# Kernel optimization log

Hardware: AMD Instinct MI355X
Metric: run time of the kernel (lower is better)

The kernel has to match this reference:

```python
import jax, jax.numpy as jnp
import numpy as np

B, N, D, T, M, V, K, HB, FF, L, H = 64, 32, 512, 8, 20, 512, 8, 16, 2048, 2, 8
SCALE = 1.0 / np.sqrt(D // H)


def _ln(x, g, b, eps=1e-5):
    m = x.mean(-1, keepdims=True)
    v = ((x - m) ** 2).mean(-1, keepdims=True)
    return (x - m) / jnp.sqrt(v + eps) * g + b


def _heads(x):
    return x.reshape(x.shape[:-1] + (H, D // H))


def setup_inputs():
    ks = iter(jax.random.split(jax.random.key(0), 60))
    def rn(shape, s=1.0):
        return jax.random.normal(next(ks), shape, jnp.float32) * s
    d = {}
    d['ego_query'] = rn((B, 1, D))
    d['agents_query'] = rn((B, N, D))
    d['bev_feature'] = rn((B, D, HB, HB))
    d['agent_states'] = rn((B, N, 8)) * 10.0
    d['agent_labels'] = rn((B, N))
    d['gt_traj'] = rn((B, T, 3))
    d['codebook'] = rn((V, 2), 0.1)
    for p in ['ego_ctx', 'bevproj', 'agent']:
        d[p + '_w'] = rn((D, D), 0.02); d[p + '_b'] = jnp.zeros((D,))
        d[p + '_g'] = jnp.ones((D,)); d[p + '_beta'] = jnp.zeros((D,))
    d['tok_emb'] = rn((V, D), 0.02)
    d['step_e'] = rn((T, D), 0.02)
    d['mode_e'] = rn((M, D), 0.02)
    d['role_e'] = rn((2, D), 0.02)
    d['bos_e'] = rn((1, D), 0.02)
    for p in ['t', 'e', 'v']:
        d[p + '_qkv_w'] = rn((L, 3 * D, D), 0.02); d[p + '_qkv_b'] = jnp.zeros((L, 3 * D))
        d[p + '_out_w'] = rn((L, D, D), 0.02); d[p + '_out_b'] = jnp.zeros((L, D))
        d[p + '_g'] = jnp.ones((L, D)); d[p + '_beta'] = jnp.zeros((L, D))
    d['ffn_w1'] = rn((L, FF, D), 0.02); d['ffn_b1'] = jnp.zeros((L, FF))
    d['ffn_w2'] = rn((L, D, FF), 0.02); d['ffn_b2'] = jnp.zeros((L, D))
    d['ffn_g'] = jnp.ones((L, D)); d['ffn_beta'] = jnp.zeros((L, D))
    d['head_w'] = rn((V, D), 0.02); d['head_b'] = jnp.zeros((V,))
    return d


def reference(ego_query, agents_query, bev_feature, agent_states, agent_labels, gt_traj, codebook,
              ego_ctx_w, ego_ctx_b, ego_ctx_g, ego_ctx_beta,
              bevproj_w, bevproj_b, bevproj_g, bevproj_beta,
              agent_w, agent_b, agent_g, agent_beta,
              tok_emb, step_e, mode_e, role_e, bos_e,
              t_qkv_w, t_qkv_b, t_out_w, t_out_b, t_g, t_beta,
              e_qkv_w, e_qkv_b, e_out_w, e_out_b, e_g, e_beta,
              v_qkv_w, v_qkv_b, v_out_w, v_out_b, v_g, v_beta,
              ffn_w1, ffn_b1, ffn_w2, ffn_b2, ffn_g, ffn_beta,
              head_w, head_b):
    Bd = ego_query.shape[0]
    P = HB * HB
    # BEV tokens [B, P, D]
    bev = jnp.transpose(bev_feature.reshape(Bd, D, P), (0, 2, 1))
    bev = jax.nn.relu(_ln(bev @ bevproj_w.T + bevproj_b, bevproj_g, bevproj_beta))
    # top-K nearest valid agents
    valid = jax.nn.sigmoid(agent_labels) > 0.05
    dist = jnp.where(valid, jnp.linalg.norm(agent_states[..., :2], axis=-1), jnp.inf)
    _, idx = jax.lax.top_k(-dist, K)
    topk_valid = jnp.take_along_axis(valid, idx, axis=1)
    agent_ctx = jnp.take_along_axis(agents_query, idx[..., None], axis=1)  # [B,K,D]
    agent_enc = jax.nn.relu(_ln(agent_ctx @ agent_w.T + agent_b, agent_g, agent_beta))
    agent_kv = agent_enc[:, :, None, :] + step_e[None, None] + role_e[1][None, None, None]  # [B,K,T,D]
    ego_base = jax.nn.relu(_ln(ego_query[:, 0] @ ego_ctx_w.T + ego_ctx_b, ego_ctx_g, ego_ctx_beta))
    # sequential codebook matching (accumulated-position NN scan, no grad)
    gt_pos = jnp.broadcast_to(gt_traj[:, None, :, :2], (Bd, M, T, 2))
    cb = jax.lax.stop_gradient(codebook)
    def cb_step(acc, pos_t):
        dsq = ((acc[:, :, None, :] + cb[None, None] - pos_t[:, :, None, :]) ** 2).sum(-1)  # [B,M,V]
        ii = jnp.argmin(dsq, axis=-1)
        return acc + cb[ii], ii
    _, idxs = jax.lax.scan(cb_step, jnp.zeros((Bd, M, 2), gt_pos.dtype),
                           jnp.moveaxis(jax.lax.stop_gradient(gt_pos), 2, 0))
    tokens = jnp.transpose(idxs, (1, 2, 0))  # [B,M,T]
    # teacher-forced input embeddings
    bos = bos_e[0][None, :] + ego_base  # [B,D]
    inp = jnp.concatenate([jnp.broadcast_to(bos[:, None, None, :], (Bd, M, 1, D)),
                           tok_emb[tokens[:, :, :-1]]], axis=2)
    ego_q = inp + step_e[None, None] + role_e[0][None, None, None] + mode_e[None, :, None, :]
    caus = jnp.triu(jnp.full((T, T), -jnp.inf, ego_q.dtype), 1)
    inv = ~topk_valid
    inv = inv & ~inv.all(axis=-1, keepdims=True)  # guard: never mask everything
    for i in range(L):
        # temporal causal self-attention over T
        qw, kw, vw = jnp.split(t_qkv_w[i], 3, 0); qb, kb, vb = jnp.split(t_qkv_b[i], 3, 0)
        Q, Kh, Vh = _heads(ego_q @ qw.T + qb), _heads(ego_q @ kw.T + kb), _heads(ego_q @ vw.T + vb)
        s = jnp.einsum('bmqhe,bmkhe->bmhqk', Q, Kh) * SCALE + caus
        o = jnp.einsum('bmhqk,bmkhe->bmqhe', jax.nn.softmax(s, -1), Vh).reshape(ego_q.shape)
        ego_q = _ln(ego_q + o @ t_out_w[i].T + t_out_b[i], t_g[i], t_beta[i])
        # ego-to-agent cross-attention (kv varies per step t)
        qw, kw, vw = jnp.split(e_qkv_w[i], 3, 0); qb, kb, vb = jnp.split(e_qkv_b[i], 3, 0)
        Q = _heads(ego_q @ qw.T + qb)  # [B,M,T,H,e]
        Kh, Vh = _heads(agent_kv @ kw.T + kb), _heads(agent_kv @ vw.T + vb)  # [B,K,T,H,e]
        s = jnp.einsum('bmthe,bkthe->bmhtk', Q, Kh) * SCALE
        s = jnp.where(inv[:, None, None, None, :], -jnp.inf, s)
        o = jnp.einsum('bmhtk,bkthe->bmthe', jax.nn.softmax(s, -1), Vh).reshape(ego_q.shape)
        ego_q = _ln(ego_q + o @ e_out_w[i].T + e_out_b[i], e_g[i], e_beta[i])
        # BEV cross-attention
        qw, kw, vw = jnp.split(v_qkv_w[i], 3, 0); qb, kb, vb = jnp.split(v_qkv_b[i], 3, 0)
        Q = _heads(ego_q @ qw.T + qb)
        Kh, Vh = _heads(bev @ kw.T + kb), _heads(bev @ vw.T + vb)  # [B,P,H,e]
        s = jnp.einsum('bmthe,bphe->bmhtp', Q, Kh) * SCALE
        o = jnp.einsum('bmhtp,bphe->bmthe', jax.nn.softmax(s, -1), Vh).reshape(ego_q.shape)
        ego_q = _ln(ego_q + o @ v_out_w[i].T + v_out_b[i], v_g[i], v_beta[i])
        # FFN
        hid = jax.nn.gelu(ego_q @ ffn_w1[i].T + ffn_b1[i], approximate=False)
        ego_q = _ln(ego_q + hid @ ffn_w2[i].T + ffn_b2[i], ffn_g[i], ffn_beta[i])
    return ego_q @ head_w.T + head_b  # token logits [B,M,T,V]
```

## Files before the change

### kernel.cpp

```cpp
#include <hip/hip_runtime.h>
#include <hip/hip_bf16.h>
#include <math.h>
#include <type_traits>

typedef __hip_bfloat16 bf16;
typedef __attribute__((ext_vector_type(8))) short bf16x8;
typedef __attribute__((ext_vector_type(4))) float f32x4;

__device__ __forceinline__ float b2f(bf16 x){ return __bfloat162float(x); }
__device__ __forceinline__ short f2s(float f){
  bf16 h = __float2bfloat16(f);
  short s; __builtin_memcpy(&s, &h, 2); return s;
}
__device__ __forceinline__ float u2f(unsigned short u){ union { unsigned int i; float f; } z; z.i = ((unsigned int)u) << 16; return z.f; }
__device__ __forceinline__ float lo2f(unsigned int u){ union { unsigned int i; float f; } z; z.i = u << 16; return z.f; }
__device__ __forceinline__ float hi2f(unsigned int u){ union { unsigned int i; float f; } z; z.i = u & 0xffff0000u; return z.f; }
__device__ __forceinline__ bf16x8 cvt8(float4 a, float4 b){
  return (bf16x8){f2s(a.x),f2s(a.y),f2s(a.z),f2s(a.w), f2s(b.x),f2s(b.y),f2s(b.z),f2s(b.w)};
}

template<typename AT, typename CT, int ACT, int BN, int RES>
__global__ __launch_bounds__(256, BN == 64 ? 2 : 1)
void k_gemm_mfma(const AT* __restrict__ A, const float* __restrict__ W,
                 const float* __restrict__ bias, CT* C,
                 const float* Rres, int rows, int Kd, int Nc)
{
  __shared__ short As[128][40];
  __shared__ short Bs[BN][40];
  constexpr int NI = BN / 32;
  int rb = blockIdx.x * 128, nb = blockIdx.y * BN;
  int tid = threadIdx.x;
  int l = tid & 63, w = tid >> 6;
  int wr = (w >> 1) * 64, wc = (w & 1) * (BN/2);
  int lr = l & 15, lk = l >> 4;
  f32x4 acc[4][NI];
  #pragma unroll
  for (int i = 0; i < 4; i++)
    #pragma unroll
    for (int j = 0; j < NI; j++)
      acc[i][j] = (f32x4){0.f, 0.f, 0.f, 0.f};
  int sr = tid >> 1;
  int sc = (tid & 1) * 16;
  bool doB = (BN == 128) || (tid < 128);
  bool doA = (rb + sr) < rows;

  float4 faA[4], fbA[4], faB[4], fbB[4];
  bf16x8 baA[2], baB[2];
  #pragma unroll
  for (int i = 0; i < 4; i++){ faA[i] = (float4){0,0,0,0}; fbA[i] = (float4){0,0,0,0};
                               faB[i] = (float4){0,0,0,0}; fbB[i] = (float4){0,0,0,0}; }
  baA[0] = baA[1] = baB[0] = baB[1] = (bf16x8){0,0,0,0,0,0,0,0};

  auto LOADS = [&](float4* fa, bf16x8* ba, float4* fb, int k0){
    if constexpr (std::is_same<AT, float>::value){
      if (doA){
        const float4* p = (const float4*)(A + (size_t)(rb + sr)*Kd + k0 + sc);
        fa[0] = p[0]; fa[1] = p[1]; fa[2] = p[2]; fa[3] = p[3];
      }
    } else {
      if (doA){
        const bf16x8* p = (const bf16x8*)((const unsigned short*)A + (size_t)(rb + sr)*Kd + k0 + sc);
        ba[0] = p[0]; ba[1] = p[1];
      }
    }
    if (doB){
      const float4* p = (const float4*)(W + (size_t)(nb + sr)*Kd + k0 + sc);
      fb[0] = p[0]; fb[1] = p[1]; fb[2] = p[2]; fb[3] = p[3];
    }
  };
  auto STOREK = [&](float4* fa, bf16x8* ba, float4* fb){
    if constexpr (std::is_same<AT, float>::value){
      *(bf16x8*)&As[sr][sc]     = cvt8(fa[0], fa[1]);
      *(bf16x8*)&As[sr][sc + 8] = cvt8(fa[2], fa[3]);
    } else {
      *(bf16x8*)&As[sr][sc]     = ba[0];
      *(bf16x8*)&As[sr][sc + 8] = ba[1];
    }
    if (doB){
      *(bf16x8*)&Bs[sr][sc]     = cvt8(fb[0], fb[1]);
      *(bf16x8*)&Bs[sr][sc + 8] = cvt8(fb[2], fb[3]);
    }
  };
  auto COMPUTE = [&](){
    bf16x8 af[4], bf_[NI];
    #pragma unroll
    for (int mi = 0; mi < 4; mi++) af[mi]  = *(const bf16x8*)&As[wr + mi*16 + lr][lk*8];
    #pragma unroll
    for (int ni = 0; ni < NI; ni++) bf_[ni] = *(const bf16x8*)&Bs[wc + ni*16 + lr][lk*8];
    #pragma unroll
    for (int mi = 0; mi < 4; mi++)
      #pragma unroll
      for (int ni = 0; ni < NI; ni++)
        acc[mi][ni] = __builtin_amdgcn_mfma_f32_16x16x32_bf16(af[mi], bf_[ni], acc[mi][ni], 0, 0, 0);
  };

  int nst = Kd >> 5;
  LOADS(faA, baA, fbA, 0);
  LOADS(faB, baB, fbB, 32);
  for (int s = 0; s < nst; s += 2){
    __syncthreads();
    STOREK(faA, baA, fbA);
    __syncthreads();
    if (s + 2 < nst) LOADS(faA, baA, fbA, (s+2)*32);
    COMPUTE();
    __syncthreads();
    STOREK(faB, baB, fbB);
    __syncthreads();
    if (s + 3 < nst) LOADS(faB, baB, fbB, (s+3)*32);
    COMPUTE();
  }

  #pragma unroll
  for (int mi = 0; mi < 4; mi++){
    #pragma unroll
    for (int ni = 0; ni < NI; ni++){
      int col = nb + wc + ni*16 + lr;
      float bs = bias[col];
      #pragma unroll
      for (int r = 0; r < 4; r++){
        int row = rb + wr + mi*16 + lk*4 + r;
        if (row < rows){
          float v = acc[mi][ni][r] + bs;
          if (RES) v += Rres[(size_t)row*Nc + col];
          if (ACT == 1) v = 0.5f*v*(1.0f + erff(v*0.70710678118654752f));
          if constexpr (std::is_same<CT, float>::value) C[(size_t)row*Nc + col] = v;
          else C[(size_t)row*Nc + col] = __float2bfloat16(v);
        }
      }
    }
  }
}

template<typename XT, typename OT>
__global__ __launch_bounds__(256) void k_ln(const XT* X, const float* R,
                                            const float* g, const float* bt,
                                            OT* out, int relu)
{
  __shared__ float red[4];
  int row = blockIdx.x, t = threadIdx.x;
  size_t base = (size_t)row * 512;
  float x0, x1;
  if constexpr (std::is_same<XT, float>::value){ x0 = X[base + t]; x1 = X[base + t + 256]; }
  else { x0 = b2f(X[base + t]); x1 = b2f(X[base + t + 256]); }
  if (R){ x0 += R[base + t]; x1 += R[base + t + 256]; }
  float v = x0 + x1;
  #pragma unroll
  for (int o = 32; o > 0; o >>= 1) v += __shfl_xor(v, o);
  if ((t & 63) == 0) red[t >> 6] = v;
  __syncthreads();
  float mean = (red[0]+red[1]+red[2]+red[3]) * (1.0f/512.0f);
  float d0 = x0 - mean, d1 = x1 - mean;
  v = d0*d0 + d1*d1;
  #pragma unroll
  for (int o = 32; o > 0; o >>= 1) v += __shfl_xor(v, o);
  __syncthreads();
  if ((t & 63) == 0) red[t >> 6] = v;
  __syncthreads();
  float var = (red[0]+red[1]+red[2]+red[3]) * (1.0f/512.0f);
  float is = 1.0f / sqrtf(var + 1e-5f);
  float y0 = d0*is*g[t] + bt[t];
  float y1 = d1*is*g[t+256] + bt[t+256];
  if (relu){ y0 = fmaxf(y0, 0.0f); y1 = fmaxf(y1, 0.0f); }
  if constexpr (std::is_same<OT, float>::value){ out[base + t] = y0; out[base + t + 256] = y1; }
  else { out[base + t] = __float2bfloat16(y0); out[base + t + 256] = __float2bfloat16(y1); }
}

__global__ void k_bev_tok(const float* __restrict__ bev, bf16* __restrict__ out){
  __shared__ float tile[32][33];
  int b = blockIdx.z;
  int d0 = blockIdx.x * 32;
  int p0 = blockIdx.y * 32;
  int tx = threadIdx.x, ty = threadIdx.y;
  #pragma unroll
  for (int i = 0; i < 4; i++){
    int d = d0 + ty + i*8;
    tile[ty + i*8][tx] = bev[((size_t)b*512 + d)*256 + p0 + tx];
  }
  __syncthreads();
  #pragma unroll
  for (int i = 0; i < 4; i++){
    int p = p0 + ty + i*8;
    out[((size_t)b*256 + p)*512 + d0 + tx] = __float2bfloat16(tile[tx][ty + i*8]);
  }
}

__global__ void k_topk(const float* __restrict__ labels, const float* __restrict__ states,
                       int* __restrict__ idxo, int* __restrict__ invo)
{
  __shared__ float dist[32];
  __shared__ int valid[32];
  int b = blockIdx.x, t = threadIdx.x;
  if (t < 32){
    float lab = labels[b*32 + t];
    float sg = 1.0f / (1.0f + expf(-lab));
    int va = sg > 0.05f;
    float x = states[((size_t)b*32 + t)*8 + 0];
    float y = states[((size_t)b*32 + t)*8 + 1];
    float d = sqrtf(__fadd_rn(__fmul_rn(x,x), __fmul_rn(y,y)));
    dist[t] = va ? d : INFINITY;
    valid[t] = va;
  }
  __syncthreads();
  if (t == 0){
    unsigned used = 0;
    int inv8[8]; int allinv = 1;
    for (int kk = 0; kk < 8; kk++){
      float best = INFINITY; int bi = -1;
      for (int i = 0; i < 32; i++){
        if (used & (1u << i)) continue;
        if (bi < 0 || dist[i] < best){ best = dist[i]; bi = i; }
      }
      used |= 1u << bi;
      idxo[b*8 + kk] = bi;
      inv8[kk] = !valid[bi];
      allinv &= inv8[kk];
    }
    for (int kk = 0; kk < 8; kk++) invo[b*8 + kk] = allinv ? 0 : inv8[kk];
  }
}

__global__ void k_gather(const float* __restrict__ aq, const int* __restrict__ idx, bf16* __restrict__ out)
{
  int rk = blockIdx.x; int b = rk >> 3;
  int src = idx[rk] & 31;
  int t = threadIdx.x;
  size_t sbase = ((size_t)(b*32 + src))*512;
  out[(size_t)rk*512 + t]       = __float2bfloat16(aq[sbase + t]);
  out[(size_t)rk*512 + t + 256] = __float2bfloat16(aq[sbase + t + 256]);
}

__global__ void k_agentkv(const float* __restrict__ enc, const float* __restrict__ step_e,
                          const float* __restrict__ role_e, bf16* __restrict__ out)
{
  int row = blockIdx.x;
  int t8 = row & 7; int bk = row >> 3;
  int tx = threadIdx.x;
  #pragma unroll
  for (int j = 0; j < 2; j++){
    int d = tx + j*256;
    out[(size_t)row*512 + d] = __float2bfloat16((enc[(size_t)bk*512 + d] + step_e[t8*512 + d]) + role_e[512 + d]);
  }
}

__global__ __launch_bounds__(64) void k_cbscan(const float* __restrict__ gt, const float* __restrict__ cb,
                                               int* __restrict__ toks)
{
  __shared__ float cbx[512], cby[512];
  int b = blockIdx.x;
  int l = threadIdx.x;
  #pragma unroll
  for (int i = 0; i < 8; i++){
    int v = l + i*64;
    cbx[v] = cb[v*2 + 0];
    cby[v] = cb[v*2 + 1];
  }
  __syncthreads();
  float ax = 0.0f, ay = 0.0f;
  for (int t = 0; t < 8; t++){
    float px = gt[(b*8 + t)*3 + 0];
    float py = gt[(b*8 + t)*3 + 1];
    float bestv = INFINITY; int besti = 0;
    #pragma unroll
    for (int i = 0; i < 8; i++){
      int v = l*8 + i;
      float dx = __fsub_rn(__fadd_rn(ax, cbx[v]), px);
      float dy = __fsub_rn(__fadd_rn(ay, cby[v]), py);
      float d = __fadd_rn(__fmul_rn(dx,dx), __fmul_rn(dy,dy));
      if (d < bestv || (d == bestv && v < besti)){ bestv = d; besti = v; }
    }
    #pragma unroll
    for (int o = 32; o > 0; o >>= 1){
      float ov = __shfl_xor(bestv, o);
      int oi = __shfl_xor(besti, o);
      if (ov < bestv || (ov == bestv && oi < besti)){ bestv = ov; besti = oi; }
    }
    ax = __fadd_rn(ax, cbx[besti]);
    ay = __fadd_rn(ay, cby[besti]);
    if (l == 0) toks[b*8 + t] = besti;
  }
}

__global__ void k_embed(const int* __restrict__ toks, const float* __restrict__ ebase,
                        const float* __restrict__ tok_emb, const float* __restrict__ step_e,
                        const float* __restrict__ mode_e, const float* __restrict__ role_e,
                        const float* __restrict__ bos_e, float* __restrict__ out)
{
  int row = blockIdx.x;
  int t = row & 7; int bm = row >> 3; int m = bm % 20; int b = bm / 20;
  int tok = (t == 0) ? 0 : (toks[b*8 + t - 1] & 511);
  int tx = threadIdx.x;
  #pragma unroll
  for (int j = 0; j < 2; j++){
    int d = tx + j*256;
    float base = (t == 0) ? (bos_e[d] + ebase[(size_t)b*512 + d])
                          : tok_emb[(size_t)tok*512 + d];
    out[(size_t)row*512 + d] = ((base + step_e[t*512 + d]) + role_e[d]) + mode_e[m*512 + d];
  }
}

__global__ __launch_bounds__(64) void k_tattn(const bf16* __restrict__ QKV, bf16* __restrict__ O)
{
  __shared__ float q[8][65], k[8][65], v[8][65], w[8][9];
  int h = blockIdx.x & 7; int bm = blockIdx.x >> 3;
  int l = threadIdx.x;
  for (int t = 0; t < 8; t++){
    size_t base = ((size_t)(bm*8 + t))*1536 + h*64 + l;
    q[t][l] = b2f(QKV[base]);
    k[t][l] = b2f(QKV[base + 512]);
    v[t][l] = b2f(QKV[base + 1024]);
  }
  __syncthreads();
  int tq = l >> 3, tk = l & 7;
  float s = -INFINITY;
  if (tk <= tq){
    float acc = 0.0f;
    #pragma unroll
    for (int e = 0; e < 64; e++) acc += q[tq][e]*k[tk][e];
    s = acc * 0.125f;
  }
  float mx = s;
  #pragma unroll
  for (int o = 1; o < 8; o <<= 1) mx = fmaxf(mx, __shfl_xor(mx, o));
  float ex = (tk <= tq) ? expf(s - mx) : 0.0f;
  float sm = ex;
  #pragma unroll
  for (int o = 1; o < 8; o <<= 1) sm += __shfl_xor(sm, o);
  w[tq][tk] = ex / sm;
  __syncthreads();
  #pragma unroll
  for (int t2 = 0; t2 < 8; t2++){
    float acc = 0.0f;
    #pragma unroll
    for (int tk2 = 0; tk2 < 8; tk2++) acc += w[t2][tk2]*v[tk2][l];
    O[((size_t)(bm*8 + t2))*512 + h*64 + l] = __float2bfloat16(acc);
  }
}

__global__ __launch_bounds__(64) void k_eattn(const bf16* __restrict__ Q, const bf16* __restrict__ KV,
                                              const int* __restrict__ inv,
                                              bf16* __restrict__ O, int row0)
{
  int blk = blockIdx.x;
  int h = blockIdx.y;
  int grow = row0 + blk;
  int t = grow & 7;
  int b = grow / 160;
  int l = threadIdx.x;
  size_t qoff = (size_t)blk*512 + h*64 + l;
  float q = b2f(Q[qoff]);
  float s[8];
  #pragma unroll
  for (int k = 0; k < 8; k++){
    float p = q * b2f(KV[((size_t)((b*8 + k)*8 + t))*1024 + h*64 + l]);
    #pragma unroll
    for (int o = 32; o > 0; o >>= 1) p += __shfl_xor(p, o);
    s[k] = p * 0.125f;
  }
  float mx = -INFINITY;
  #pragma unroll
  for (int k = 0; k < 8; k++){
    if (inv[b*8 + k]) s[k] = -INFINITY;
    mx = fmaxf(mx, s[k]);
  }
  float sum = 0.0f, w[8];
  #pragma unroll
  for (int k = 0; k < 8; k++){ w[k] = expf(s[k] - mx); sum += w[k]; }
  float rs = 1.0f / sum;
  float acc = 0.0f;
  #pragma unroll
  for (int k = 0; k < 8; k++)
    acc += (w[k]*rs) * b2f(KV[((size_t)((b*8 + k)*8 + t))*1024 + 512 + h*64 + l]);
  O[qoff] = __float2bfloat16(acc);
}

__global__ __launch_bounds__(256, 2) void k_vattn(const bf16* __restrict__ Q, const bf16* __restrict__ KV,
                                                  bf16* __restrict__ O)
{
  __shared__ unsigned short Ks[256][72];
  __shared__ unsigned short Vt[64][264];
  __shared__ float red[2][2][16];
  unsigned short (*P_lds)[264] = (unsigned short (*)[264])&Ks[0][0];

  int bl = blockIdx.x, h = blockIdx.y, qz = blockIdx.z;
  int tid = threadIdx.x;
  const unsigned short* KVr = (const unsigned short*)KV;

  {
    const uint4* ksrc = (const uint4*)&KVr[((size_t)(bl*256 + tid))*1024 + h*64];
    const uint4* vsrc = (const uint4*)&KVr[((size_t)(bl*256 + tid))*1024 + 512 + h*64];
    #pragma unroll
    for (int i = 0; i < 8; i++){
      uint4 kx = ksrc[i];
      *(uint4*)&Ks[tid][i*8] = kx;
    }
    #pragma unroll
    for (int i = 0; i < 8; i++){
      uint4 vx = vsrc[i];
      unsigned short vs[8];
      __builtin_memcpy(vs, &vx, 16);
      #pragma unroll
      for (int j = 0; j < 8; j++) Vt[i*8 + j][tid] = vs[j];
    }
  }
  __syncthreads();

  int w = tid >> 6, l = tid & 63, lr = l & 15, lk = l >> 4;
  int mt = w >> 1, ch = w & 1;

  int qrow = bl*160 + qz*32 + mt*16 + lr;
  const unsigned short* Qr = (const unsigned short*)Q;
  bf16x8 qf0 = *(const bf16x8*)&Qr[(size_t)qrow*512 + h*64 + lk*8];
  bf16x8 qf1 = *(const bf16x8*)&Qr[(size_t)qrow*512 + h*64 + 32 + lk*8];

  f32x4 sacc[8];
  #pragma unroll
  for (int nt = 0; nt < 8; nt++) sacc[nt] = (f32x4){0.f,0.f,0.f,0.f};
  #pragma unroll
  for (int nt = 0; nt < 8; nt++){
    int key0 = ch*128 + nt*16 + lr;
    bf16x8 kf0 = *(const bf16x8*)&Ks[key0][lk*8];
    bf16x8 kf1 = *(const bf16x8*)&Ks[key0][32 + lk*8];
    sacc[nt] = __builtin_amdgcn_mfma_f32_16x16x32_bf16(qf0, kf0, sacc[nt], 0, 0, 0);
    sacc[nt] = __builtin_amdgcn_mfma_f32_16x16x32_bf16(qf1, kf1, sacc[nt], 0, 0, 0);
  }

  float rmax[4] = {-INFINITY, -INFINITY, -INFINITY, -INFINITY};
  #pragma unroll
  for (int nt = 0; nt < 8; nt++)
    #pragma unroll
    for (int r = 0; r < 4; r++){
      float v = sacc[nt][r] * 0.125f;
      sacc[nt][r] = v;
      rmax[r] = fmaxf(rmax[r], v);
    }
  #pragma unroll
  for (int r = 0; r < 4; r++){
    #pragma unroll
    for (int o = 1; o < 16; o <<= 1) rmax[r] = fmaxf(rmax[r], __shfl_xor(rmax[r], o));
  }
  if (lr == 0){
    #pragma unroll
    for (int r = 0; r < 4; r++) red[mt][ch][lk*4 + r] = rmax[r];
  }
  __syncthreads();
  float m4[4];
  #pragma unroll
  for (int r = 0; r < 4; r++) m4[r] = fmaxf(red[mt][0][lk*4 + r], red[mt][1][lk*4 + r]);
  float rsum[4] = {0.f, 0.f, 0.f, 0.f};
  #pragma unroll
  for (int nt = 0; nt < 8; nt++){
    #pragma unroll
    for (int r = 0; r < 4; r++){
      float e = expf(sacc[nt][r] - m4[r]);
      rsum[r] += e;
      P_lds[mt*16 + lk*4 + r][ch*128 + nt*16 + lr] = (unsigned short)f2s(e);
    }
  }
  #pragma unroll
  for (int r = 0; r < 4; r++){
    #pragma unroll
    for (int o = 1; o < 16; o <<= 1) rsum[r] += __shfl_xor(rsum[r], o);
  }
  __syncthreads();
  if (lr == 0){
    #pragma unroll
    for (int r = 0; r < 4; r++) red[mt][ch][lk*4 + r] = rsum[r];
  }
  __syncthreads();
  float rcp4[4];
  #pragma unroll
  for (int r = 0; r < 4; r++) rcp4[r] = 1.0f / (red[mt][0][lk*4 + r] + red[mt][1][lk*4 + r]);

  f32x4 oacc0 = (f32x4){0.f,0.f,0.f,0.f};
  f32x4 oacc1 = (f32x4){0.f,0.f,0.f,0.f};
  #pragma unroll
  for (int kk = 0; kk < 8; kk++){
    bf16x8 pf  = *(const bf16x8*)&P_lds[mt*16 + lr][kk*32 + lk*8];
    bf16x8 vf0 = *(const bf16x8*)&Vt[ch*32 + lr][kk*32 + lk*8];
    bf16x8 vf1 = *(const bf16x8*)&Vt[ch*32 + 16 + lr][kk*32 + lk*8];
    oacc0 = __builtin_amdgcn_mfma_f32_16x16x32_bf16(pf, vf0, oacc0, 0, 0, 0);
    oacc1 = __builtin_amdgcn_mfma_f32_16x16x32_bf16(pf, vf1, oacc1, 0, 0, 0);
  }

  {
    size_t obase = ((size_t)(bl*160 + qz*32 + mt*16 + lk*4))*512 + h*64 + ch*32 + lr;
    #pragma unroll
    for (int r = 0; r < 4; r++){
      O[obase + (size_t)r*512]      = __float2bfloat16(oacc0[r] * rcp4[r]);
      O[obase + (size_t)r*512 + 16] = __float2bfloat16(oacc1[r] * rcp4[r]);
    }
  }
}

extern "C" void kernel_launch(void* const* d_in, const int* in_sizes, int n_in,
                              void* d_out, int out_size, void* d_ws, size_t ws_size,
                              hipStream_t stream)
{
  (void)in_sizes; (void)n_in; (void)out_size;
  const float* ego_query    = (const float*)d_in[0];
  const float* agents_query = (const float*)d_in[1];
  const float* bev_feature  = (const float*)d_in[2];
  const float* agent_states = (const float*)d_in[3];
  const float* agent_labels = (const float*)d_in[4];
  const float* gt_traj      = (const float*)d_in[5];
  const float* codebook     = (const float*)d_in[6];
  const float* ego_ctx_w    = (const float*)d_in[7];
  const float* ego_ctx_b    = (const float*)d_in[8];
  const float* ego_ctx_g    = (const float*)d_in[9];
  const float* ego_ctx_beta = (const float*)d_in[10];
  const float* bevproj_w    = (const float*)d_in[11];
  const float* bevproj_b    = (const float*)d_in[12];
  const float* bevproj_g    = (const float*)d_in[13];
  const float* bevproj_beta = (const float*)d_in[14];
  const float* agent_w      = (const float*)d_in[15];
  const float* agent_b      = (const float*)d_in[16];
  const float* agent_g      = (const float*)d_in[17];
  const float* agent_beta   = (const float*)d_in[18];
  const float* tok_emb      = (const float*)d_in[19];
  const float* step_e       = (const float*)d_in[20];
  const float* mode_e       = (const float*)d_in[21];
  const float* role_e       = (const float*)d_in[22];
  const float* bos_e        = (const float*)d_in[23];
  const float* t_qkv_w      = (const float*)d_in[24];
  const float* t_qkv_b      = (const float*)d_in[25];
  const float* t_out_w      = (const float*)d_in[26];
  const float* t_out_b      = (const float*)d_in[27];
  const float* t_g          = (const float*)d_in[28];
  const float* t_beta       = (const float*)d_in[29];
  const float* e_qkv_w      = (const float*)d_in[30];
  const float* e_qkv_b      = (const float*)d_in[31];
  const float* e_out_w      = (const float*)d_in[32];
  const float* e_out_b      = (const float*)d_in[33];
  const float* e_g          = (const float*)d_in[34];
  const float* e_beta       = (const float*)d_in[35];
  const float* v_qkv_w      = (const float*)d_in[36];
  const float* v_qkv_b      = (const float*)d_in[37];
  const float* v_out_w      = (const float*)d_in[38];
  const float* v_out_b      = (const float*)d_in[39];
  const float* v_g          = (const float*)d_in[40];
  const float* v_beta       = (const float*)d_in[41];
  const float* ffn_w1       = (const float*)d_in[42];
  const float* ffn_b1       = (const float*)d_in[43];
  const float* ffn_w2       = (const float*)d_in[44];
  const float* ffn_b2       = (const float*)d_in[45];
  const float* ffn_g        = (const float*)d_in[46];
  const float* ffn_beta     = (const float*)d_in[47];
  const float* head_w       = (const float*)d_in[48];
  const float* head_b       = (const float*)d_in[49];

  const size_t NEEDED       = 46274560;
  const size_t NEEDED_BIG   = 67248128;
  const size_t NEEDED_BIG2  = 100800512;
  if (ws_size < NEEDED) return;
  bool big  = ws_size >= NEEDED_BIG;
  bool big2 = ws_size >= NEEDED_BIG2;
  int RC  = big ? 10240 : 5120;
  int NCH = big ? 1 : 2;

  char* WB = (char*)d_ws;
  bf16*  bevtok = (bf16*)(WB + 0);
  bf16*  akv    = (bf16*)(WB + 16777216);
  float* ebase  = (float*)(WB + 20971520);
  char*  ARENA  = WB + 21102592;
  bf16*  KVb    = (bf16*)(WB + 37879808);
  bf16*  KVbig  = (bf16*)(WB + 67239936);
  size_t tk0    = big2 ? 100794368 : (big ? 67239936 : 46268416);
  int*   toks   = (int*)(WB + tk0);
  int*   idxb   = (int*)(WB + tk0 + 2048);
  int*   invb   = (int*)(WB + tk0 + 4096);
  size_t oe_off = big ? 31457280 : 5242880;

  float* egoq = (float*)d_out;

  #define GEMM(AT,CT,ACT,BN,RES, Ap,Wp,Bp,Cp,Rp, R,K,N) \
    k_gemm_mfma<AT,CT,ACT,BN,RES><<<dim3(((R)+127)/128,(N)/(BN)),256,0,stream>>>(Ap,Wp,Bp,Cp,Rp,R,K,N)

  {
    bf16* raw = (bf16*)ARENA;
    k_bev_tok<<<dim3(16, 8, 64), dim3(32, 8), 0, stream>>>(bev_feature, raw);
    GEMM(bf16,bf16,0,64,0, raw, bevproj_w, bevproj_b, bevtok, nullptr, 16384, 512, 512);
    k_ln<bf16,bf16><<<16384, 256, 0, stream>>>(bevtok, nullptr, bevproj_g, bevproj_beta, bevtok, 1);
  }

  GEMM(float,float,0,64,0, ego_query, ego_ctx_w, ego_ctx_b, (float*)ARENA, nullptr, 64, 512, 512);
  k_ln<float,float><<<64, 256, 0, stream>>>((float*)ARENA, nullptr, ego_ctx_g, ego_ctx_beta, ebase, 1);

  k_topk<<<64, 64, 0, stream>>>(agent_labels, agent_states, idxb, invb);
  {
    bf16*  gat = (bf16*)ARENA;
    float* enc = (float*)(ARENA + 524288);
    k_gather<<<512, 256, 0, stream>>>(agents_query, idxb, gat);
    GEMM(bf16,float,0,64,0, gat, agent_w, agent_b, enc, nullptr, 512, 512, 512);
    k_ln<float,float><<<512, 256, 0, stream>>>(enc, nullptr, agent_g, agent_beta, enc, 1);
    k_agentkv<<<4096, 256, 0, stream>>>(enc, step_e, role_e, akv);
  }

  k_cbscan<<<64, 64, 0, stream>>>(gt_traj, codebook, toks);
  k_embed<<<10240, 256, 0, stream>>>(toks, ebase, tok_emb, step_e, mode_e, role_e, bos_e, egoq);

  for (int i = 0; i < 2; i++){
    {
      bf16* QKV = (bf16*)ARENA;
      bf16* Ot  = big ? (bf16*)(ARENA + oe_off) : KVb;
      for (int c = 0; c < NCH; c++){
        float* eg = egoq + (size_t)c*RC*512;
        GEMM(float,bf16,0,128,0, eg, t_qkv_w + (size_t)i*786432, t_qkv_b + i*1536, QKV, nullptr, RC, 512, 1536);
        k_tattn<<<RC, 64, 0, stream>>>(QKV, Ot);
        GEMM(bf16,float,0,64,1, Ot, t_out_w + (size_t)i*262144, t_out_b + i*512, eg, eg, RC, 512, 512);
      }
      k_ln<float,float><<<10240, 256, 0, stream>>>(egoq, nullptr, t_g + i*512, t_beta + i*512, egoq, 0);
    }
    {
      const float* eqw = e_qkv_w + (size_t)i*786432;
      const float* eqb = e_qkv_b + i*1536;
      bf16* Qe = (bf16*)ARENA;
      bf16* Oe = (bf16*)(ARENA + oe_off);
      GEMM(bf16,bf16,0,64,0, akv, eqw + 262144, eqb + 512, KVb, nullptr, 4096, 512, 1024);
      for (int c = 0; c < NCH; c++){
        float* eg = egoq + (size_t)c*RC*512;
        GEMM(float,bf16,0,64,0, eg, eqw, eqb, Qe, nullptr, RC, 512, 512);
        k_eattn<<<dim3(RC, 8), 64, 0, stream>>>(Qe, KVb, invb, Oe, c*RC);
        GEMM(bf16,float,0,64,1, Oe, e_out_w + (size_t)i*262144, e_out_b + i*512, eg, eg, RC, 512, 512);
      }
      k_ln<float,float><<<10240, 256, 0, stream>>>(egoq, nullptr, e_g + i*512, e_beta + i*512, egoq, 0);
    }
    {
      const float* vqw = v_qkv_w + (size_t)i*786432;
      const float* vqb = v_qkv_b + i*1536;
      if (big2){
        bf16* Qv = (bf16*)ARENA;
        bf16* Ov = (bf16*)(ARENA + 10485760);
        GEMM(bf16,bf16,0,64,0, bevtok, vqw + 262144, vqb + 512, KVbig, nullptr, 16384, 512, 1024);
        GEMM(float,bf16,0,64,0, egoq, vqw, vqb, Qv, nullptr, 10240, 512, 512);
        k_vattn<<<dim3(64, 8, 5), 256, 0, stream>>>(Qv, KVbig, Ov);
        GEMM(bf16,float,0,64,1, Ov, v_out_w + (size_t)i*262144, v_out_b + i*512, egoq, egoq, 10240, 512, 512);
      } else {
        bf16* Qv = (bf16*)ARENA;
        bf16* Ov = (bf16*)(ARENA + 2621440);
        for (int gidx = 0; gidx < 4; gidx++){
          float* eg = egoq + (size_t)gidx*2560*512;
          GEMM(bf16,bf16,0,64,0, bevtok + (size_t)gidx*4096*512, vqw + 262144, vqb + 512, KVb, nullptr, 4096, 512, 1024);
          GEMM(float,bf16,0,64,0, eg, vqw, vqb, Qv, nullptr, 2560, 512, 512);
          k_vattn<<<dim3(16, 8, 5), 256, 0, stream>>>(Qv, KVb, Ov);
          GEMM(bf16,float,0,64,1, Ov, v_out_w + (size_t)i*262144, v_out_b + i*512, eg, eg, 2560, 512, 512);
        }
      }
      k_ln<float,float><<<10240, 256, 0, stream>>>(egoq, nullptr, v_g + i*512, v_beta + i*512, egoq, 0);
    }
    {
      bf16* hid = (bf16*)ARENA;
      for (int c = 0; c < NCH; c++){
        float* eg = egoq + (size_t)c*RC*512;
        GEMM(float,bf16,1,128,0, eg, ffn_w1 + (size_t)i*1048576, ffn_b1 + i*2048, hid, nullptr, RC, 512, 2048);
        GEMM(bf16,float,0,64,1, hid, ffn_w2 + (size_t)i*1048576, ffn_b2 + i*512, eg, eg, RC, 2048, 512);
      }
      if (i == 0){
        k_ln<float,float><<<10240, 256, 0, stream>>>(egoq, nullptr, ffn_g, ffn_beta, egoq, 0);
      } else {
        k_ln<float,bf16><<<10240, 256, 0, stream>>>(egoq, nullptr, ffn_g + 512, ffn_beta + 512, (bf16*)ARENA, 0);
      }
    }
  }

  GEMM(bf16,float,0,64,0, (bf16*)ARENA, head_w, head_b, (float*)d_out, nullptr, 10240, 512, 512);
  #undef GEMM
}
```

Baseline: 1.169 ms.

## Enlarge GEMM row tile to 256 and simplify to single-stage register prefetch

The MFMA GEMM tile grows from 128 to 256 rows. Each wave now computes 128 rows with 8x NI accumulators, and each thread loads one full A row per K-step. The two-stage ping-pong register prefetch is replaced by a single prefetch buffer, and the B-fragment load moves inside the inner loop. The aim is more weight reuse per block and fewer redundant weight loads. In exchange it doubles accumulator register pressure, which may lower occupancy given the launch bounds. It also halves the grid size for the small row counts (64, 512), leaving fewer blocks to fill the CUs.

```diff
diff --git a/kernel.cpp b/kernel.cpp
--- a/kernel.cpp
+++ b/kernel.cpp
@@ -13,8 +13,6 @@
   short s; __builtin_memcpy(&s, &h, 2); return s;
 }
 __device__ __forceinline__ float u2f(unsigned short u){ union { unsigned int i; float f; } z; z.i = ((unsigned int)u) << 16; return z.f; }
-__device__ __forceinline__ float lo2f(unsigned int u){ union { unsigned int i; float f; } z; z.i = u << 16; return z.f; }
-__device__ __forceinline__ float hi2f(unsigned int u){ union { unsigned int i; float f; } z; z.i = u & 0xffff0000u; return z.f; }
 __device__ __forceinline__ bf16x8 cvt8(float4 a, float4 b){
   return (bf16x8){f2s(a.x),f2s(a.y),f2s(a.z),f2s(a.w), f2s(b.x),f2s(b.y),f2s(b.z),f2s(b.w)};
 }
@@ -25,93 +23,94 @@
                  const float* __restrict__ bias, CT* C,
                  const float* Rres, int rows, int Kd, int Nc)
 {
-  __shared__ short As[128][40];
+  __shared__ short As[256][40];
   __shared__ short Bs[BN][40];
   constexpr int NI = BN / 32;
-  int rb = blockIdx.x * 128, nb = blockIdx.y * BN;
+  int rb = blockIdx.x * 256, nb = blockIdx.y * BN;
   int tid = threadIdx.x;
   int l = tid & 63, w = tid >> 6;
-  int wr = (w >> 1) * 64, wc = (w & 1) * (BN/2);
+  int wr = (w >> 1) * 128, wc = (w & 1) * (BN/2);
   int lr = l & 15, lk = l >> 4;
-  f32x4 acc[4][NI];
-  #pragma unroll
-  for (int i = 0; i < 4; i++)
+  f32x4 acc[8][NI];
+  #pragma unroll
+  for (int i = 0; i < 8; i++)
     #pragma unroll
     for (int j = 0; j < NI; j++)
       acc[i][j] = (f32x4){0.f, 0.f, 0.f, 0.f};
-  int sr = tid >> 1;
-  int sc = (tid & 1) * 16;
-  bool doB = (BN == 128) || (tid < 128);
-  bool doA = (rb + sr) < rows;
-
-  float4 faA[4], fbA[4], faB[4], fbB[4];
-  bf16x8 baA[2], baB[2];
-  #pragma unroll
-  for (int i = 0; i < 4; i++){ faA[i] = (float4){0,0,0,0}; fbA[i] = (float4){0,0,0,0};
-                               faB[i] = (float4){0,0,0,0}; fbB[i] = (float4){0,0,0,0}; }
-  baA[0] = baA[1] = baB[0] = baB[1] = (bf16x8){0,0,0,0,0,0,0,0};
-
-  auto LOADS = [&](float4* fa, bf16x8* ba, float4* fb, int k0){
+  int sra = tid;
+  int srb = tid / (256/BN);
+  int scb = (tid % (256/BN)) * (BN/8);
+  bool doA = (rb + sra) < rows;
+
+  float4 fa[8]; bf16x8 ba[4]; float4 fb[NI];
+  #pragma unroll
+  for (int i = 0; i < 8; i++) fa[i] = (float4){0,0,0,0};
+  #pragma unroll
+  for (int i = 0; i < 4; i++) ba[i] = (bf16x8){0,0,0,0,0,0,0,0};
+  #pragma unroll
+  for (int i = 0; i < NI; i++) fb[i] = (float4){0,0,0,0};
+
+  auto LOADS = [&](int k0){
     if constexpr (std::is_same<AT, float>::value){
       if (doA){
-        const float4* p = (const float4*)(A + (size_t)(rb + sr)*Kd + k0 + sc);
-        fa[0] = p[0]; fa[1] = p[1]; fa[2] = p[2]; fa[3] = p[3];
+        const float4* p = (const float4*)(A + (size_t)(rb + sra)*Kd + k0);
+        #pragma unroll
+        for (int i = 0; i < 8; i++) fa[i] = p[i];
       }
     } else {
       if (doA){
-        const bf16x8* p = (const bf16x8*)((const unsigned short*)A + (size_t)(rb + sr)*Kd + k0 + sc);
-        ba[0] = p[0]; ba[1] = p[1];
-      }
-    }
-    if (doB){
-      const float4* p = (const float4*)(W + (size_t)(nb + sr)*Kd + k0 + sc);
-      fb[0] = p[0]; fb[1] = p[1]; fb[2] = p[2]; fb[3] = p[3];
+        const bf16x8* p = (const bf16x8*)((const unsigned short*)A + (size_t)(rb + sra)*Kd + k0);
+        #pragma unroll
+        for (int i = 0; i < 4; i++) ba[i] = p[i];
+      }
+    }
+    {
+      const float4* p = (const float4*)(W + (size_t)(nb + srb)*Kd + k0 + scb);
+      #pragma unroll
+      for (int i = 0; i < NI; i++) fb[i] = p[i];
     }
   };
-  auto STOREK = [&](float4* fa, bf16x8* ba, float4* fb){
+  auto STOREK = [&](){
     if constexpr (std::is_same<AT, float>::value){
-      *(bf16x8*)&As[sr][sc]     = cvt8(fa[0], fa[1]);
-      *(bf16x8*)&As[sr][sc + 8] = cvt8(fa[2], fa[3]);
+      *(bf16x8*)&As[sra][0]  = cvt8(fa[0], fa[1]);
+      *(bf16x8*)&As[sra][8]  = cvt8(fa[2], fa[3]);
+      *(bf16x8*)&As[sra][16] = cvt8(fa[4], fa[5]);
+      *(bf16x8*)&As[sra][24] = cvt8(fa[6], fa[7]);
     } else {
-      *(bf16x8*)&As[sr][sc]     = ba[0];
-      *(bf16x8*)&As[sr][sc + 8] = ba[1];
-    }
-    if (doB){
-      *(bf16x8*)&Bs[sr][sc]     = cvt8(fb[0], fb[1]);
-      *(bf16x8*)&Bs[sr][sc + 8] = cvt8(fb[2], fb[3]);
-    }
+      *(bf16x8*)&As[sra][0]  = ba[0];
+      *(bf16x8*)&As[sra][8]  = ba[1];
+      *(bf16x8*)&As[sra][16] = ba[2];
+      *(bf16x8*)&As[sra][24] = ba[3];
+    }
+    #pragma unroll
+    for (int i = 0; i < NI/2; i++)
+      *(bf16x8*)&Bs[srb][scb + i*8] = cvt8(fb[2*i], fb[2*i + 1]);
+    if (NI == 2 && (BN/8) == 8){  }
   };
   auto COMPUTE = [&](){
-    bf16x8 af[4], bf_[NI];
-    #pragma unroll
-    for (int mi = 0; mi < 4; mi++) af[mi]  = *(const bf16x8*)&As[wr + mi*16 + lr][lk*8];
-    #pragma unroll
-    for (int ni = 0; ni < NI; ni++) bf_[ni] = *(const bf16x8*)&Bs[wc + ni*16 + lr][lk*8];
-    #pragma unroll
-    for (int mi = 0; mi < 4; mi++)
+    #pragma unroll
+    for (int mi = 0; mi < 8; mi++){
+      bf16x8 af = *(const bf16x8*)&As[wr + mi*16 + lr][lk*8];
       #pragma unroll
-      for (int ni = 0; ni < NI; ni++)
-        acc[mi][ni] = __builtin_amdgcn_mfma_f32_16x16x32_bf16(af[mi], bf_[ni], acc[mi][ni], 0, 0, 0);
+      for (int ni = 0; ni < NI; ni++){
+        bf16x8 bfr = *(const bf16x8*)&Bs[wc + ni*16 + lr][lk*8];
+        acc[mi][ni] = __builtin_amdgcn_mfma_f32_16x16x32_bf16(af, bfr, acc[mi][ni], 0, 0, 0);
+      }
+    }
   };
 
   int nst = Kd >> 5;
-  LOADS(faA, baA, fbA, 0);
-  LOADS(faB, baB, fbB, 32);
-  for (int s = 0; s < nst; s += 2){
+  LOADS(0);
+  for (int s = 0; s < nst; s++){
     __syncthreads();
-    STOREK(faA, baA, fbA);
+    STOREK();
     __syncthreads();
-    if (s + 2 < nst) LOADS(faA, baA, fbA, (s+2)*32);
+    if (s + 1 < nst) LOADS((s + 1) * 32);
     COMPUTE();
-    __syncthreads();
-    STOREK(faB, baB, fbB);
-    __syncthreads();
-    if (s + 3 < nst) LOADS(faB, baB, fbB, (s+3)*32);
-    COMPUTE();
-  }
-
-  #pragma unroll
-  for (int mi = 0; mi < 4; mi++){
+  }
+
+  #pragma unroll
+  for (int mi = 0; mi < 8; mi++){
     #pragma unroll
     for (int ni = 0; ni < NI; ni++){
       int col = nb + wc + ni*16 + lr;
@@ -573,7 +572,7 @@
   float* egoq = (float*)d_out;
 
   #define GEMM(AT,CT,ACT,BN,RES, Ap,Wp,Bp,Cp,Rp, R,K,N) \
-    k_gemm_mfma<AT,CT,ACT,BN,RES><<<dim3(((R)+127)/128,(N)/(BN)),256,0,stream>>>(Ap,Wp,Bp,Cp,Rp,R,K,N)
+    k_gemm_mfma<AT,CT,ACT,BN,RES><<<dim3(((R)+255)/256,(N)/(BN)),256,0,stream>>>(Ap,Wp,Bp,Cp,Rp,R,K,N)
 
   {
     bf16* raw = (bf16*)ARENA;
```

Measured after the change: 1.594 ms. 1.36x slower.
